# Kernel optimization log

Hardware: AMD Instinct MI355X
Metric: run time of the kernel (lower is better)

Reference implementation:

```python
import jax, jax.numpy as jnp
import numpy as np

N_NODES = 100000
N_EDGES = 1600000
IN_DIM, HID_DIM, OUT_DIM = 128, 128, 64


def setup_inputs() -> dict:
    key = jax.random.key(0)
    ks = jax.random.split(key, 8)
    x = jax.random.normal(ks[0], (N_NODES, IN_DIM), dtype=jnp.float32)
    edge_index = jax.random.randint(ks[1], (2, N_EDGES), 0, N_NODES, dtype=jnp.int64)
    s1 = 1.0 / np.sqrt(IN_DIM)
    s2 = 1.0 / np.sqrt(HID_DIM)
    return {
        "x": x,
        "edge_index": edge_index,
        "W1l": jax.random.normal(ks[2], (IN_DIM, HID_DIM), dtype=jnp.float32) * s1,
        "b1": jnp.zeros((HID_DIM,), dtype=jnp.float32),
        "W1r": jax.random.normal(ks[3], (IN_DIM, HID_DIM), dtype=jnp.float32) * s1,
        "W2l": jax.random.normal(ks[4], (HID_DIM, OUT_DIM), dtype=jnp.float32) * s2,
        "b2": jnp.zeros((OUT_DIM,), dtype=jnp.float32),
        "W2r": jax.random.normal(ks[5], (HID_DIM, OUT_DIM), dtype=jnp.float32) * s2,
    }


def _sage_conv(h, src, dst, n_nodes, Wl, bl, Wr):
    # mean-aggregate neighbor messages src -> dst, then linear + root linear
    msg = h[src]                                               # [E, d]
    summed = jax.ops.segment_sum(msg, dst, num_segments=n_nodes)
    cnt = jax.ops.segment_sum(jnp.ones((src.shape[0],), h.dtype), dst,
                              num_segments=n_nodes)
    aggr = summed / jnp.maximum(cnt, 1.0)[:, None]             # [N, d]
    return aggr @ Wl + bl + h @ Wr                             # [N, d_out]


def reference(x, edge_index, W1l, b1, W1r, W2l, b2, W2r):
    src, dst = edge_index[0], edge_index[1]
    n = x.shape[0]
    h = jax.nn.relu(_sage_conv(x, src, dst, n, W1l, b1, W1r))
    # dropout is identity in eval mode (training=False)
    return _sage_conv(h, src, dst, n, W2l, b2, W2r)
```

## Files before the change

### kernel.cpp

```cpp
#include <hip/hip_runtime.h>
#include <hip/hip_bf16.h>
#include <stdint.h>

#define N_NODES 100000
#define N_EDGES 1600000
#define IN_DIM 128
#define HID_DIM 128
#define OUT_DIM 64
#define NBUCKET 391
#define NBE 391
#define ECHUNK 4096
#define HM (NBUCKET * NBE)
#define NB_SCAN 150
#define SENTINEL N_NODES
#define PCAP 6144
#define GEMM_ROWBLKS 782
#define GEMM_GRID (GEMM_ROWBLKS * 2)

typedef __bf16 bf16x8 __attribute__((ext_vector_type(8)));
typedef float f32x4 __attribute__((ext_vector_type(4)));
typedef float f32x2 __attribute__((ext_vector_type(2)));

__device__ __forceinline__ uint16_t f_to_bf16(float f) {
    uint32_t u = __float_as_uint(f);
    u += 0x7fffu + ((u >> 16) & 1u);
    return (uint16_t)(u >> 16);
}
__device__ __forceinline__ uint32_t pack_bf16x2(float lo, float hi) {
    return (uint32_t)f_to_bf16(lo) | ((uint32_t)f_to_bf16(hi) << 16);
}


__global__ __launch_bounds__(256) void prep_k(const int* __restrict__ dst,
                                              const float* __restrict__ x,
                                              const float* __restrict__ W1l,
                                              const float* __restrict__ W1r,
                                              const float* __restrict__ W2l,
                                              const float* __restrict__ W2r,
                                              int* __restrict__ hist,
                                              uint16_t* __restrict__ xb,
                                              uint32_t* __restrict__ xf8,
                                              uint16_t* __restrict__ wT1,
                                              uint16_t* __restrict__ wT2) {
    __shared__ int lh[NBUCKET];
    int blk = blockIdx.x, t = threadIdx.x;
    if (blk < NBE) {
        for (int i = t; i < NBUCKET; i += 256) lh[i] = 0;
        __syncthreads();
        int e0 = blk * ECHUNK;
        int e1 = e0 + ECHUNK; if (e1 > N_EDGES) e1 = N_EDGES;
        for (int e = e0 + t; e < e1; e += 256) atomicAdd(&lh[dst[e] >> 8], 1);
        __syncthreads();
        for (int i = t; i < NBUCKET; i += 256) hist[i * NBE + blk] = lh[i];
    } else if (blk < NBE + 6250) {
        int i = (blk - NBE) * 256 + t;
        if (blk == NBE && t < 32) xf8[N_NODES * 32 + t] = 0u;
        if (i >= N_NODES * IN_DIM / 8) return;
        const float4* xv = (const float4*)x;
        float4 v0 = xv[2 * i], v1 = xv[2 * i + 1];
        union { uint16_t u[8]; uint4 q; } o;
        o.u[0] = f_to_bf16(v0.x); o.u[1] = f_to_bf16(v0.y);
        o.u[2] = f_to_bf16(v0.z); o.u[3] = f_to_bf16(v0.w);
        o.u[4] = f_to_bf16(v1.x); o.u[5] = f_to_bf16(v1.y);
        o.u[6] = f_to_bf16(v1.z); o.u[7] = f_to_bf16(v1.w);
        ((uint4*)xb)[i] = o.q;
        int p0 = __builtin_amdgcn_cvt_pk_fp8_f32(v0.x, v0.y, 0, false);
        p0 = __builtin_amdgcn_cvt_pk_fp8_f32(v0.z, v0.w, p0, true);
        int p1 = __builtin_amdgcn_cvt_pk_fp8_f32(v1.x, v1.y, 0, false);
        p1 = __builtin_amdgcn_cvt_pk_fp8_f32(v1.z, v1.w, p1, true);
        uint2 w2; w2.x = (uint32_t)p0; w2.y = (uint32_t)p1;
        ((uint2*)xf8)[i] = w2;
    } else {
        int i = (blk - NBE - 6250) * 256 + t;
        if (i < 128 * 256) {
            int n = i >> 8, k = i & 255;
            float v = (k < 128) ? W1l[k * 128 + n] : W1r[(k - 128) * 128 + n];
            wT1[i] = f_to_bf16(v);
        } else {
            int j = i - 128 * 256;
            if (j < 128 * 128) {
                int n = j >> 7, k = j & 127;
                float v = (n < 64) ? W2l[k * 64 + n] : W2r[k * 64 + (n - 64)];
                wT2[j] = f_to_bf16(v);
            }
        }
    }
}


__global__ void scan1_k(int* __restrict__ data, int* __restrict__ partials, int n) {
    __shared__ int sm[256];
    int tid = threadIdx.x;
    int base = blockIdx.x * 1024 + tid * 4;
    int v0 = 0, v1 = 0, v2 = 0, v3 = 0;
    if (base + 0 < n) v0 = data[base + 0];
    if (base + 1 < n) v1 = data[base + 1];
    if (base + 2 < n) v2 = data[base + 2];
    if (base + 3 < n) v3 = data[base + 3];
    int tot = v0 + v1 + v2 + v3;
    sm[tid] = tot;
    __syncthreads();
    int val = tot;
    for (int off = 1; off < 256; off <<= 1) {
        int x = (tid >= off) ? sm[tid - off] : 0;
        __syncthreads();
        val += x;
        sm[tid] = val;
        __syncthreads();
    }
    int excl = val - tot;
    if (tid == 255) partials[blockIdx.x] = val;
    if (base + 0 < n) data[base + 0] = excl;
    if (base + 1 < n) data[base + 1] = excl + v0;
    if (base + 2 < n) data[base + 2] = excl + v0 + v1;
    if (base + 3 < n) data[base + 3] = excl + v0 + v1 + v2;
}

__global__ void scan3_k(int* __restrict__ data, const int* __restrict__ partials, int n) {
    __shared__ int sm[256];
    __shared__ int sp[256];
    int t = threadIdx.x;
    int v = (t < NB_SCAN) ? partials[t] : 0;
    sm[t] = v;
    __syncthreads();
    int val = v;
    for (int off = 1; off < 256; off <<= 1) {
        int x = (t >= off) ? sm[t - off] : 0;
        __syncthreads();
        val += x;
        sm[t] = val;
        __syncthreads();
    }
    sp[t] = val - v;
    __syncthreads();
    int i = blockIdx.x * 256 + t;
    if (i < n) data[i] += sp[i >> 10];
}

__global__ __launch_bounds__(256) void scatter2_k(const int* __restrict__ src,
                                                  const int* __restrict__ dst,
                                                  const int* __restrict__ hoff,
                                                  uint32_t* __restrict__ packed) {
    __shared__ int loff[NBUCKET];
    int blk = blockIdx.x, t = threadIdx.x;
    for (int i = t; i < NBUCKET; i += 256) loff[i] = hoff[i * NBE + blk];
    __syncthreads();
    int e0 = blk * ECHUNK;
    int e1 = e0 + ECHUNK; if (e1 > N_EDGES) e1 = N_EDGES;
    for (int e = e0 + t; e < e1; e += 256) {
        int d = dst[e];
        int pos = atomicAdd(&loff[d >> 8], 1);
        packed[pos] = ((uint32_t)src[e] << 8) | (uint32_t)(d & 255);
    }
}


__global__ __launch_bounds__(256) void finalize_k(const uint32_t* __restrict__ packed,
                                                  const int* __restrict__ hoff,
                                                  int* __restrict__ csr,
                                                  int* __restrict__ deg,
                                                  int* __restrict__ prowst) {
    __shared__ int lhist[256];
    __shared__ int ssc[256];
    __shared__ int lcur[256];
    __shared__ int s_pcnt;
    __shared__ uint32_t lpk[PCAP];
    __shared__ int lcsr[PCAP];
    int b = blockIdx.x, t = threadIdx.x;
    int base = hoff[b * NBE];
    int next = (b + 1 < NBUCKET) ? hoff[(b + 1) * NBE] : N_EDGES;
    int cnt = next - base;
    lhist[t] = 0;
    __syncthreads();
    bool fit = (cnt <= PCAP);
    if (fit) {
        for (int i = t; i < cnt; i += 256) {
            uint32_t pk = packed[base + i];
            lpk[i] = pk;
            atomicAdd(&lhist[pk & 255u], 1);
        }
    } else {
        for (int i = t; i < cnt; i += 256) atomicAdd(&lhist[packed[base + i] & 255u], 1);
    }
    __syncthreads();
    int d = lhist[t];
    int pd = (d + 7) & ~7;
    ssc[t] = pd;
    __syncthreads();
    int val = pd;
    for (int off = 1; off < 256; off <<= 1) {
        int x = (t >= off) ? ssc[t - off] : 0;
        __syncthreads();
        val += x;
        ssc[t] = val;
        __syncthreads();
    }
    int excl = val - pd;
    lcur[t] = excl;
    if (t == 255) s_pcnt = val;
    int node = (b << 8) + t;
    if (node < N_NODES) { deg[node] = d; prowst[node] = b * PCAP + excl; }
    __syncthreads();
    int pcnt = s_pcnt;
    int cbase = b * PCAP;
    if (fit && pcnt <= PCAP) {
        for (int i = t; i < pcnt; i += 256) lcsr[i] = SENTINEL;
        __syncthreads();
        for (int i = t; i < cnt; i += 256) {
            uint32_t pk = lpk[i];
            int pos = atomicAdd(&lcur[pk & 255u], 1);
            lcsr[pos] = (int)(pk >> 8);
        }
        __syncthreads();
        for (int i = t; i < pcnt; i += 256) csr[cbase + i] = lcsr[i];
    } else {
        int lim = pcnt < PCAP ? pcnt : PCAP;
        for (int i = t; i < lim; i += 256) csr[cbase + i] = SENTINEL;
        __syncthreads();
        for (int i = t; i < cnt; i += 256) {
            uint32_t pk = packed[base + i];
            int pos = atomicAdd(&lcur[pk & 255u], 1);
            if (pos < PCAP) csr[cbase + pos] = (int)(pk >> 8);
        }
    }
}


__global__ void aggregate_k(const int* __restrict__ csr, const int* __restrict__ prowst,
                            const int* __restrict__ deg,
                            const uint32_t* __restrict__ inf8, uint32_t* __restrict__ out2) {
    int gw = (blockIdx.x * blockDim.x + threadIdx.x) >> 6;
    int lane = threadIdx.x & 63;
    int c = lane & 31, p = lane >> 5;
    int node = 2 * gw + p;
    int start = prowst[node];
    int d = deg[node];
    int pd = (d + 7) & ~7;
    f32x2 s01 = (f32x2){0.f, 0.f}, s23 = (f32x2){0.f, 0.f};
    for (int j = 0; j < pd; j += 8) {
        uint32_t q[8];
#pragma unroll
        for (int u = 0; u < 8; u++) {
            int s = csr[start + j + u];
            q[u] = inf8[(s << 5) + c];
        }
#pragma unroll
        for (int u = 0; u < 8; u++) {
            s01 += __builtin_amdgcn_cvt_pk_f32_fp8((int)q[u], false);
            s23 += __builtin_amdgcn_cvt_pk_f32_fp8((int)q[u], true);
        }
    }
    float inv = 1.0f / (float)(d > 0 ? d : 1);
    uint2 o;
    o.x = pack_bf16x2(s01[0] * inv, s01[1] * inv);
    o.y = pack_bf16x2(s23[0] * inv, s23[1] * inv);
    ((uint2*)out2)[node * 32 + c] = o;
}


__global__ __launch_bounds__(256, 4) void gemm1_k(const uint16_t* __restrict__ ab,
                                                  const uint16_t* __restrict__ xb,
                                                  const uint16_t* __restrict__ wT1,
                                                  const float* __restrict__ b1,
                                                  uint16_t* __restrict__ hb) {
    __shared__ uint16_t lw[64 * 256];
    int t = threadIdx.x;
    int nh = blockIdx.x & 1;
    int rowblk = blockIdx.x >> 1;
    {
        const uint4* gsrc = (const uint4*)wT1;
        uint4* ldst = (uint4*)lw;
        for (int i = t; i < 2048; i += 256) {
            int r = i >> 5, cc = i & 31;
            ldst[(r << 5) + (cc ^ (r & 31))] = gsrc[((nh * 64 + r) << 5) + cc];
        }
    }
    __syncthreads();

    int wave = t >> 6;
    int lane = t & 63;
    int m0 = rowblk * 128 + wave * 32;
    int mr = lane & 15, quad = lane >> 4;

    const uint16_t* A1[2];
    const uint16_t* A2[2];
#pragma unroll
    for (int s = 0; s < 2; s++) {
        int row = m0 + s * 16 + mr;
        if (row > N_NODES - 1) row = N_NODES - 1;
        A1[s] = ab + (size_t)row * 128 + quad * 8;
        A2[s] = xb + (size_t)row * 128 + quad * 8;
    }

    f32x4 acc[4][2];
#pragma unroll
    for (int nt = 0; nt < 4; nt++)
#pragma unroll
        for (int s = 0; s < 2; s++) acc[nt][s] = (f32x4){0.f, 0.f, 0.f, 0.f};

#pragma unroll
    for (int kt = 0; kt < 8; kt++) {
        bf16x8 av[2];
#pragma unroll
        for (int s = 0; s < 2; s++) {
            const uint16_t* ap = (kt < 4) ? (A1[s] + kt * 32) : (A2[s] + (kt - 4) * 32);
            av[s] = *reinterpret_cast<const bf16x8*>(ap);
        }
#pragma unroll
        for (int nt = 0; nt < 4; nt++) {
            int brow = nt * 16 + mr;
            int chunk = kt * 4 + quad;
            const uint16_t* bp = lw + (brow << 8) + ((chunk ^ (brow & 31)) << 3);
            bf16x8 b = *reinterpret_cast<const bf16x8*>(bp);
#pragma unroll
            for (int s = 0; s < 2; s++)
                acc[nt][s] = __builtin_amdgcn_mfma_f32_16x16x32_bf16(av[s], b, acc[nt][s], 0, 0, 0);
        }
    }

    __syncthreads();
#pragma unroll
    for (int nt = 0; nt < 4; nt++) {
        int col = nt * 16 + mr;
        float bias = b1[nh * 64 + col];
#pragma unroll
        for (int s = 0; s < 2; s++) {
#pragma unroll
            for (int r = 0; r < 4; r++) {
                int lrow = wave * 32 + s * 16 + quad * 4 + r;
                float v = acc[nt][s][r] + bias;
                v = v > 0.f ? v : 0.f;
                lw[lrow * 72 + col] = f_to_bf16(v);
            }
        }
    }
    __syncthreads();
    {
        int rows0 = rowblk * 128;
        for (int c2 = t; c2 < 1024; c2 += 256) {
            int r = c2 >> 3, part = c2 & 7;
            int grow = rows0 + r;
            if (grow < N_NODES) {
                uint4 v = *reinterpret_cast<const uint4*>(lw + r * 72 + part * 8);
                *reinterpret_cast<uint4*>(hb + (size_t)grow * 128 + nh * 64 + part * 8) = v;
            }
        }
    }
}


__global__ __launch_bounds__(256, 4) void gemm2_k(const uint16_t* __restrict__ hb,
                                                  const uint16_t* __restrict__ wT2,
                                                  const float* __restrict__ b2,
                                                  uint8_t* __restrict__ g,
                                                  float* __restrict__ z) {
    __shared__ uint16_t lw[64 * 128];
    int t = threadIdx.x;
    int nh = blockIdx.x & 1;
    int rowblk = blockIdx.x >> 1;
    if (blockIdx.x == 0 && t < 16)
        ((uint32_t*)(g + (size_t)N_NODES * 64))[t] = 0u;
    {
        const uint4* gsrc = (const uint4*)wT2;
        uint4* ldst = (uint4*)lw;
        for (int i = t; i < 1024; i += 256) {
            int r = i >> 4, cc = i & 15;
            ldst[(r << 4) + (cc ^ (r & 15))] = gsrc[((nh * 64 + r) << 4) + cc];
        }
    }
    __syncthreads();

    int wave = t >> 6;
    int lane = t & 63;
    int m0 = rowblk * 128 + wave * 32;
    int mr = lane & 15, quad = lane >> 4;

    const uint16_t* A[2];
#pragma unroll
    for (int s = 0; s < 2; s++) {
        int row = m0 + s * 16 + mr;
        if (row > N_NODES - 1) row = N_NODES - 1;
        A[s] = hb + (size_t)row * 128 + quad * 8;
    }

    f32x4 acc[4][2];
#pragma unroll
    for (int nt = 0; nt < 4; nt++)
#pragma unroll
        for (int s = 0; s < 2; s++) acc[nt][s] = (f32x4){0.f, 0.f, 0.f, 0.f};

#pragma unroll
    for (int kt = 0; kt < 4; kt++) {
        bf16x8 av[2];
#pragma unroll
        for (int s = 0; s < 2; s++)
            av[s] = *reinterpret_cast<const bf16x8*>(A[s] + kt * 32);
#pragma unroll
        for (int nt = 0; nt < 4; nt++) {
            int brow = nt * 16 + mr;
            int chunk = kt * 4 + quad;
            const uint16_t* bp = lw + (brow << 7) + ((chunk ^ (brow & 15)) << 3);
            bf16x8 b = *reinterpret_cast<const bf16x8*>(bp);
#pragma unroll
            for (int s = 0; s < 2; s++)
                acc[nt][s] = __builtin_amdgcn_mfma_f32_16x16x32_bf16(av[s], b, acc[nt][s], 0, 0, 0);
        }
    }

    if (nh == 0) {
        __syncthreads();
        uint8_t* ep8 = (uint8_t*)lw;
#pragma unroll
        for (int nt = 0; nt < 4; nt++) {
            int col = nt * 16 + mr;
#pragma unroll
            for (int s = 0; s < 2; s++) {
#pragma unroll
                for (int r = 0; r < 4; r++) {
                    int lrow = wave * 32 + s * 16 + quad * 4 + r;
                    float v = acc[nt][s][r];
                    int pk = __builtin_amdgcn_cvt_pk_fp8_f32(v, v, 0, false);
                    ep8[lrow * 80 + col] = (uint8_t)(pk & 0xff);
                }
            }
        }
        __syncthreads();
        int rows0 = rowblk * 128;
        for (int c2 = t; c2 < 512; c2 += 256) {
            int r = c2 >> 2, part = c2 & 3;
            int grow = rows0 + r;
            if (grow < N_NODES) {
                uint4 v = *reinterpret_cast<const uint4*>(ep8 + r * 80 + part * 16);
                *reinterpret_cast<uint4*>(g + (size_t)grow * 64 + part * 16) = v;
            }
        }
    } else {
#pragma unroll
        for (int nt = 0; nt < 4; nt++) {
            int col = nt * 16 + mr;
            float bias = b2[col];
#pragma unroll
            for (int s = 0; s < 2; s++) {
#pragma unroll
                for (int r = 0; r < 4; r++) {
                    int row = m0 + s * 16 + quad * 4 + r;
                    if (row < N_NODES)
                        z[(size_t)row * 64 + col] = acc[nt][s][r] + bias;
                }
            }
        }
    }
}


__global__ void agg2_k(const int* __restrict__ csr, const int* __restrict__ prowst,
                       const int* __restrict__ deg,
                       const uint32_t* __restrict__ g4, const float* __restrict__ z,
                       float* __restrict__ out) {
    int gw = (blockIdx.x * blockDim.x + threadIdx.x) >> 6;
    int lane = threadIdx.x & 63;
    int c = lane & 15, q4 = lane >> 4;
    int node = 4 * gw + q4;
    int start = prowst[node];
    int d = deg[node];
    int pd = (d + 7) & ~7;
    f32x2 s01 = (f32x2){0.f, 0.f}, s23 = (f32x2){0.f, 0.f};
    for (int j = 0; j < pd; j += 8) {
        uint32_t q[8];
#pragma unroll
        for (int u = 0; u < 8; u++) {
            int s = csr[start + j + u];
            q[u] = g4[(s << 4) + c];
        }
#pragma unroll
        for (int u = 0; u < 8; u++) {
            s01 += __builtin_amdgcn_cvt_pk_f32_fp8((int)q[u], false);
            s23 += __builtin_amdgcn_cvt_pk_f32_fp8((int)q[u], true);
        }
    }
    float inv = 1.0f / (float)(d > 0 ? d : 1);
    float4 zz = ((const float4*)z)[node * 16 + c];
    float4 o;
    o.x = s01[0] * inv + zz.x;
    o.y = s01[1] * inv + zz.y;
    o.z = s23[0] * inv + zz.z;
    o.w = s23[1] * inv + zz.w;
    ((float4*)out)[node * 16 + c] = o;
}


extern "C" void kernel_launch(void* const* d_in, const int* in_sizes, int n_in,
                              void* d_out, int out_size, void* d_ws, size_t ws_size,
                              hipStream_t stream) {
    const float* x   = (const float*)d_in[0];
    const int*  ei   = (const int*)d_in[1];
    const float* W1l = (const float*)d_in[2];
    const float* b1  = (const float*)d_in[3];
    const float* W1r = (const float*)d_in[4];
    const float* W2l = (const float*)d_in[5];
    const float* b2  = (const float*)d_in[6];
    const float* W2r = (const float*)d_in[7];
    float* out = (float*)d_out;

    const int* srcv = ei;
    const int* dstv = ei + N_EDGES;

    char* ws = (char*)d_ws;
    int*      deg      = (int*)(ws + 0);
    int*      prowst   = (int*)(ws + 401408);
    int*      partials = (int*)(ws + 802816);
    int*      csr      = (int*)(ws + 1209344);
    uint16_t* wT1      = (uint16_t*)(ws + 13809664);
    uint16_t* wT2      = (uint16_t*)(ws + 13875200);
    uint16_t* xb       = (uint16_t*)(ws + 13907968);
    char*     abreg    = (ws + 39507968);
    uint16_t* hb       = (uint16_t*)(ws + 65107968);
    uint16_t* ab       = (uint16_t*)abreg;
    float*    z        = (float*)abreg;
    uint8_t*  g        = (uint8_t*)xb;
    uint32_t* packed   = (uint32_t*)hb;
    int*      hoff     = (int*)(ws + 65107968 + 6400000);
    uint32_t* xf8      = (uint32_t*)(ws + 65107968 + 7013376);

    prep_k<<<NBE + 6250 + 192, 256, 0, stream>>>(dstv, x, W1l, W1r, W2l, W2r,
                                                 hoff, xb, xf8, wT1, wT2);
    scan1_k<<<NB_SCAN, 256, 0, stream>>>(hoff, partials, HM);
    scan3_k<<<(HM + 255) / 256, 256, 0, stream>>>(hoff, partials, HM);
    scatter2_k<<<NBE, 256, 0, stream>>>(srcv, dstv, hoff, packed);
    finalize_k<<<NBUCKET, 256, 0, stream>>>(packed, hoff, csr, deg, prowst);

    aggregate_k<<<12500, 256, 0, stream>>>(csr, prowst, deg, xf8, (uint32_t*)ab);
    gemm1_k<<<GEMM_GRID, 256, 0, stream>>>(ab, xb, wT1, b1, hb);

    gemm2_k<<<GEMM_GRID, 256, 0, stream>>>(hb, wT2, b2, g, z);
    agg2_k<<<6250, 256, 0, stream>>>(csr, prowst, deg, (const uint32_t*)g, z, out);
}
```

Baseline: 159.5 us.

## Replace histogram-scan-scatter CSR build with atomic bucket reservation in prep kernel

Edge bucketing now happens in a single pass inside the prep kernel. Each block builds a local histogram of destination buckets, reserves space in fixed-capacity per-bucket slots with global atomics, then scatters packed edges directly. This removes the two scan kernels and the separate scatter kernel, cutting launches and a global prefix-sum pass. In exchange, edge order within each bucket becomes nondeterministic, and any edges beyond PCAP per bucket are silently dropped. An extra memset is also added.

```diff
diff --git a/kernel.cpp b/kernel.cpp
--- a/kernel.cpp
+++ b/kernel.cpp
@@ -8,10 +8,8 @@
 #define HID_DIM 128
 #define OUT_DIM 64
 #define NBUCKET 391
-#define NBE 391
-#define ECHUNK 4096
-#define HM (NBUCKET * NBE)
-#define NB_SCAN 150
+#define SC_NB 98
+#define SC_CHUNK 16384
 #define SENTINEL N_NODES
 #define PCAP 6144
 #define GEMM_ROWBLKS 782
@@ -31,30 +29,43 @@
 }
 
 
-__global__ __launch_bounds__(256) void prep_k(const int* __restrict__ dst,
+__global__ __launch_bounds__(256) void prep_k(const int* __restrict__ src,
+                                              const int* __restrict__ dst,
                                               const float* __restrict__ x,
                                               const float* __restrict__ W1l,
                                               const float* __restrict__ W1r,
                                               const float* __restrict__ W2l,
                                               const float* __restrict__ W2r,
-                                              int* __restrict__ hist,
+                                              int* __restrict__ bcur,
+                                              uint32_t* __restrict__ packed,
                                               uint16_t* __restrict__ xb,
                                               uint32_t* __restrict__ xf8,
                                               uint16_t* __restrict__ wT1,
                                               uint16_t* __restrict__ wT2) {
     __shared__ int lh[NBUCKET];
     int blk = blockIdx.x, t = threadIdx.x;
-    if (blk < NBE) {
+    if (blk < SC_NB) {
         for (int i = t; i < NBUCKET; i += 256) lh[i] = 0;
         __syncthreads();
-        int e0 = blk * ECHUNK;
-        int e1 = e0 + ECHUNK; if (e1 > N_EDGES) e1 = N_EDGES;
+        int e0 = blk * SC_CHUNK;
+        int e1 = e0 + SC_CHUNK; if (e1 > N_EDGES) e1 = N_EDGES;
         for (int e = e0 + t; e < e1; e += 256) atomicAdd(&lh[dst[e] >> 8], 1);
         __syncthreads();
-        for (int i = t; i < NBUCKET; i += 256) hist[i * NBE + blk] = lh[i];
-    } else if (blk < NBE + 6250) {
-        int i = (blk - NBE) * 256 + t;
-        if (blk == NBE && t < 32) xf8[N_NODES * 32 + t] = 0u;
+        for (int i = t; i < NBUCKET; i += 256) {
+            int c = lh[i];
+            lh[i] = c ? atomicAdd(&bcur[i], c) : 0;
+        }
+        __syncthreads();
+        for (int e = e0 + t; e < e1; e += 256) {
+            int d = dst[e];
+            int b = d >> 8;
+            int pos = atomicAdd(&lh[b], 1);
+            if (pos < PCAP)
+                packed[b * PCAP + pos] = ((uint32_t)src[e] << 8) | (uint32_t)(d & 255);
+        }
+    } else if (blk < SC_NB + 6250) {
+        int i = (blk - SC_NB) * 256 + t;
+        if (blk == SC_NB && t < 32) xf8[N_NODES * 32 + t] = 0u;
         if (i >= N_NODES * IN_DIM / 8) return;
         const float4* xv = (const float4*)x;
         float4 v0 = xv[2 * i], v1 = xv[2 * i + 1];
@@ -71,7 +82,7 @@
         uint2 w2; w2.x = (uint32_t)p0; w2.y = (uint32_t)p1;
         ((uint2*)xf8)[i] = w2;
     } else {
-        int i = (blk - NBE - 6250) * 256 + t;
+        int i = (blk - SC_NB - 6250) * 256 + t;
         if (i < 128 * 256) {
             int n = i >> 8, k = i & 255;
             float v = (k < 128) ? W1l[k * 128 + n] : W1r[(k - 128) * 128 + n];
@@ -88,75 +99,8 @@
 }
 
 
-__global__ void scan1_k(int* __restrict__ data, int* __restrict__ partials, int n) {
-    __shared__ int sm[256];
-    int tid = threadIdx.x;
-    int base = blockIdx.x * 1024 + tid * 4;
-    int v0 = 0, v1 = 0, v2 = 0, v3 = 0;
-    if (base + 0 < n) v0 = data[base + 0];
-    if (base + 1 < n) v1 = data[base + 1];
-    if (base + 2 < n) v2 = data[base + 2];
-    if (base + 3 < n) v3 = data[base + 3];
-    int tot = v0 + v1 + v2 + v3;
-    sm[tid] = tot;
-    __syncthreads();
-    int val = tot;
-    for (int off = 1; off < 256; off <<= 1) {
-        int x = (tid >= off) ? sm[tid - off] : 0;
-        __syncthreads();
-        val += x;
-        sm[tid] = val;
-        __syncthreads();
-    }
-    int excl = val - tot;
-    if (tid == 255) partials[blockIdx.x] = val;
-    if (base + 0 < n) data[base + 0] = excl;
-    if (base + 1 < n) data[base + 1] = excl + v0;
-    if (base + 2 < n) data[base + 2] = excl + v0 + v1;
-    if (base + 3 < n) data[base + 3] = excl + v0 + v1 + v2;
-}
-
-__global__ void scan3_k(int* __restrict__ data, const int* __restrict__ partials, int n) {
-    __shared__ int sm[256];
-    __shared__ int sp[256];
-    int t = threadIdx.x;
-    int v = (t < NB_SCAN) ? partials[t] : 0;
-    sm[t] = v;
-    __syncthreads();
-    int val = v;
-    for (int off = 1; off < 256; off <<= 1) {
-        int x = (t >= off) ? sm[t - off] : 0;
-        __syncthreads();
-        val += x;
-        sm[t] = val;
-        __syncthreads();
-    }
-    sp[t] = val - v;
-    __syncthreads();
-    int i = blockIdx.x * 256 + t;
-    if (i < n) data[i] += sp[i >> 10];
-}
-
-__global__ __launch_bounds__(256) void scatter2_k(const int* __restrict__ src,
-                                                  const int* __restrict__ dst,
-                                                  const int* __restrict__ hoff,
-                                                  uint32_t* __restrict__ packed) {
-    __shared__ int loff[NBUCKET];
-    int blk = blockIdx.x, t = threadIdx.x;
-    for (int i = t; i < NBUCKET; i += 256) loff[i] = hoff[i * NBE + blk];
-    __syncthreads();
-    int e0 = blk * ECHUNK;
-    int e1 = e0 + ECHUNK; if (e1 > N_EDGES) e1 = N_EDGES;
-    for (int e = e0 + t; e < e1; e += 256) {
-        int d = dst[e];
-        int pos = atomicAdd(&loff[d >> 8], 1);
-        packed[pos] = ((uint32_t)src[e] << 8) | (uint32_t)(d & 255);
-    }
-}
-
-
 __global__ __launch_bounds__(256) void finalize_k(const uint32_t* __restrict__ packed,
-                                                  const int* __restrict__ hoff,
+                                                  const int* __restrict__ bcur,
                                                   int* __restrict__ csr,
                                                   int* __restrict__ deg,
                                                   int* __restrict__ prowst) {
@@ -167,20 +111,15 @@
     __shared__ uint32_t lpk[PCAP];
     __shared__ int lcsr[PCAP];
     int b = blockIdx.x, t = threadIdx.x;
-    int base = hoff[b * NBE];
-    int next = (b + 1 < NBUCKET) ? hoff[(b + 1) * NBE] : N_EDGES;
-    int cnt = next - base;
+    int base = b * PCAP;
+    int cnt = bcur[b];
+    if (cnt > PCAP) cnt = PCAP;
     lhist[t] = 0;
     __syncthreads();
-    bool fit = (cnt <= PCAP);
-    if (fit) {
-        for (int i = t; i < cnt; i += 256) {
-            uint32_t pk = packed[base + i];
-            lpk[i] = pk;
-            atomicAdd(&lhist[pk & 255u], 1);
-        }
-    } else {
-        for (int i = t; i < cnt; i += 256) atomicAdd(&lhist[packed[base + i] & 255u], 1);
+    for (int i = t; i < cnt; i += 256) {
+        uint32_t pk = packed[base + i];
+        lpk[i] = pk;
+        atomicAdd(&lhist[pk & 255u], 1);
     }
     __syncthreads();
     int d = lhist[t];
@@ -203,7 +142,7 @@
     __syncthreads();
     int pcnt = s_pcnt;
     int cbase = b * PCAP;
-    if (fit && pcnt <= PCAP) {
+    if (pcnt <= PCAP) {
         for (int i = t; i < pcnt; i += 256) lcsr[i] = SENTINEL;
         __syncthreads();
         for (int i = t; i < cnt; i += 256) {
@@ -218,7 +157,7 @@
         for (int i = t; i < lim; i += 256) csr[cbase + i] = SENTINEL;
         __syncthreads();
         for (int i = t; i < cnt; i += 256) {
-            uint32_t pk = packed[base + i];
+            uint32_t pk = lpk[i];
             int pos = atomicAdd(&lcur[pk & 255u], 1);
             if (pos < PCAP) csr[cbase + pos] = (int)(pk >> 8);
         }
@@ -508,7 +447,7 @@
     char* ws = (char*)d_ws;
     int*      deg      = (int*)(ws + 0);
     int*      prowst   = (int*)(ws + 401408);
-    int*      partials = (int*)(ws + 802816);
+    int*      bcur     = (int*)(ws + 802816);
     int*      csr      = (int*)(ws + 1209344);
     uint16_t* wT1      = (uint16_t*)(ws + 13809664);
     uint16_t* wT2      = (uint16_t*)(ws + 13875200);
@@ -519,15 +458,12 @@
     float*    z        = (float*)abreg;
     uint8_t*  g        = (uint8_t*)xb;
     uint32_t* packed   = (uint32_t*)hb;
-    int*      hoff     = (int*)(ws + 65107968 + 6400000);
-    uint32_t* xf8      = (uint32_t*)(ws + 65107968 + 7013376);
-
-    prep_k<<<NBE + 6250 + 192, 256, 0, stream>>>(dstv, x, W1l, W1r, W2l, W2r,
-                                                 hoff, xb, xf8, wT1, wT2);
-    scan1_k<<<NB_SCAN, 256, 0, stream>>>(hoff, partials, HM);
-    scan3_k<<<(HM + 255) / 256, 256, 0, stream>>>(hoff, partials, HM);
-    scatter2_k<<<NBE, 256, 0, stream>>>(srcv, dstv, hoff, packed);
-    finalize_k<<<NBUCKET, 256, 0, stream>>>(packed, hoff, csr, deg, prowst);
+    uint32_t* xf8      = (uint32_t*)(ws + 65107968 + 9609216);
+
+    hipMemsetAsync(bcur, 0, NBUCKET * sizeof(int), stream);
+    prep_k<<<SC_NB + 6250 + 192, 256, 0, stream>>>(srcv, dstv, x, W1l, W1r, W2l, W2r,
+                                                   bcur, packed, xb, xf8, wT1, wT2);
+    finalize_k<<<NBUCKET, 256, 0, stream>>>(packed, bcur, csr, deg, prowst);
 
     aggregate_k<<<12500, 256, 0, stream>>>(csr, prowst, deg, xf8, (uint32_t*)ab);
     gemm1_k<<<GEMM_GRID, 256, 0, stream>>>(ab, xb, wT1, b1, hb);
```

Result: slower. 191.0 us (+19.8%).
